# Kernel tuning notes

Measured on AMD Instinct MI355X. Metric: run time of the kernel, lower is better.

Reference implementation:

```python
import jax, jax.numpy as jnp
import numpy as np

B, N = 4, 5000


def setup_inputs() -> dict:
    key = jax.random.key(0)
    k1, k2, k3, k4 = jax.random.split(key, 4)
    param_b = jax.random.uniform(k1, (B, 1, 1), dtype=jnp.float32)
    param_g = jax.random.uniform(k2, (B, 1, 1), dtype=jnp.float32)
    mob = jax.random.uniform(k3, (B, N, N), dtype=jnp.float32)
    SIR = jax.random.uniform(k4, (B, N, 3), dtype=jnp.float32)
    return {"param_b": param_b, "param_g": param_g, "mob": mob, "SIR": SIR}


def reference(param_b, param_g, mob, SIR):
    # SIR: [B, N, 3]; mob: [B, N, N]
    S = SIR[..., 0:1]  # [B, N, 1]
    I = SIR[..., 1:2]
    R = SIR[..., 2:3]
    pop = (S + I + R)[..., 0]  # [B, N], pop_i broadcast along row i of mob
    Iv = I[..., 0]             # [B, N]
    # torch: (mob/pop * I_row).sum(1)  -> sum_i mob[b,i,j] * I_i / pop_i
    term_col = jnp.einsum('bij,bi->bj', mob, Iv / pop)
    # torch: (mob/pop * I_col).sum(2)  -> (1/pop_i) * sum_j mob[b,i,j] * I_j
    term_row = jnp.einsum('bij,bj->bi', mob, Iv) / pop
    propagation = (term_col + term_row)[..., None]  # [B, N, 1]
    I_new = param_b * propagation
    R_t = I * param_g + R
    I_t = I + I_new - I * param_g
    S_t = S - I_new
    return jnp.concatenate((I_new, S_t, I_t, R_t), axis=-1)  # [B, N, 4]
```

## Files before the change

### kernel.cpp

```cpp
#include <hip/hip_runtime.h>


constexpr int B  = 4;
constexpr int N  = 5000;
constexpr int NT = 256;
constexpr int ROWS_MAX = 80;

typedef float f32x4 __attribute__((ext_vector_type(4)));

__global__ __launch_bounds__(NT, 4) void sir_phase1(
    const float* __restrict__ mob, const float* __restrict__ SIR,
    float* __restrict__ ws_row, float* __restrict__ ws_col, int P)
{
    const int b = blockIdx.y;
    const int k = blockIdx.x;
    const int t = threadIdx.x;

    __shared__ float red[ROWS_MAX][4];

    const float* sir_b = SIR + (size_t)b * N * 3;

    f32x4 iv[5];
    #pragma unroll
    for (int kk = 0; kk < 5; ++kk) {
        const int j4 = 4 * t + 1024 * kk;
        if (kk < 4 || t < 226) {
            iv[kk][0] = sir_b[(j4 + 0) * 3 + 1];
            iv[kk][1] = sir_b[(j4 + 1) * 3 + 1];
            iv[kk][2] = sir_b[(j4 + 2) * 3 + 1];
            iv[kk][3] = sir_b[(j4 + 3) * 3 + 1];
        } else {
            iv[kk] = (f32x4)0.f;
        }
    }

    f32x4 col[5];
    #pragma unroll
    for (int kk = 0; kk < 5; ++kk) col[kk] = (f32x4)0.f;

    const float* mob_b = mob + (size_t)b * N * N;

    int r = 0;
    for (int i = k; i < N; i += P, ++r) {
        const float s  = sir_b[i * 3 + 0];
        const float ii = sir_b[i * 3 + 1];
        const float rr = sir_b[i * 3 + 2];
        const float w  = ii / (s + ii + rr);

        const float* mrow = mob_b + (size_t)i * N;
        float rp = 0.f;
        #pragma unroll
        for (int kk = 0; kk < 4; ++kk) {
            const f32x4 m = __builtin_nontemporal_load(
                reinterpret_cast<const f32x4*>(mrow + 4 * t + 1024 * kk));
            rp = fmaf(m[0], iv[kk][0], rp);
            rp = fmaf(m[1], iv[kk][1], rp);
            rp = fmaf(m[2], iv[kk][2], rp);
            rp = fmaf(m[3], iv[kk][3], rp);
            col[kk][0] = fmaf(m[0], w, col[kk][0]);
            col[kk][1] = fmaf(m[1], w, col[kk][1]);
            col[kk][2] = fmaf(m[2], w, col[kk][2]);
            col[kk][3] = fmaf(m[3], w, col[kk][3]);
        }
        if (t < 226) {
            const f32x4 m = __builtin_nontemporal_load(
                reinterpret_cast<const f32x4*>(mrow + 4 * t + 4096));
            rp = fmaf(m[0], iv[4][0], rp);
            rp = fmaf(m[1], iv[4][1], rp);
            rp = fmaf(m[2], iv[4][2], rp);
            rp = fmaf(m[3], iv[4][3], rp);
            col[4][0] = fmaf(m[0], w, col[4][0]);
            col[4][1] = fmaf(m[1], w, col[4][1]);
            col[4][2] = fmaf(m[2], w, col[4][2]);
            col[4][3] = fmaf(m[3], w, col[4][3]);
        }
        #pragma unroll
        for (int off = 32; off > 0; off >>= 1)
            rp += __shfl_xor(rp, off, 64);
        if ((t & 63) == 0) red[r][t >> 6] = rp;
    }
    __syncthreads();

    for (int q = t; q < r; q += NT) {
        const int i = k + P * q;
        ws_row[(size_t)b * N + i] = red[q][0] + red[q][1] + red[q][2] + red[q][3];
    }

    float* cp = ws_col + ((size_t)b * P + k) * N;
    #pragma unroll
    for (int kk = 0; kk < 4; ++kk)
        *reinterpret_cast<f32x4*>(cp + 4 * t + 1024 * kk) = col[kk];
    if (t < 226)
        *reinterpret_cast<f32x4*>(cp + 4 * t + 4096) = col[4];
}

__global__ __launch_bounds__(256) void sir_phase2(
    const float* __restrict__ ws_row, const float* __restrict__ ws_col,
    const float* __restrict__ SIR, const float* __restrict__ pb,
    const float* __restrict__ pg, float* __restrict__ out, int P)
{
    const int b = blockIdx.y;
    const int j = blockIdx.x * 256 + threadIdx.x;
    if (j >= N) return;

    const float* base = ws_col + (size_t)b * P * N + j;
    float cs = 0.f;
    #pragma unroll 8
    for (int p = 0; p < P; ++p) cs += base[(size_t)p * N];

    const float s  = SIR[((size_t)b * N + j) * 3 + 0];
    const float ii = SIR[((size_t)b * N + j) * 3 + 1];
    const float rr = SIR[((size_t)b * N + j) * 3 + 2];
    const float pop = s + ii + rr;
    const float tr = ws_row[(size_t)b * N + j] / pop;
    const float inew = pb[b] * (cs + tr);
    const float ig = ii * pg[b];

    f32x4 o;
    o[0] = inew;
    o[1] = s - inew;
    o[2] = ii + inew - ig;
    o[3] = ig + rr;
    *reinterpret_cast<f32x4*>(out + ((size_t)b * N + j) * 4) = o;
}

extern "C" void kernel_launch(void* const* d_in, const int* in_sizes, int n_in,
                              void* d_out, int out_size, void* d_ws, size_t ws_size,
                              hipStream_t stream)
{
    const float* pb  = (const float*)d_in[0];
    const float* pg  = (const float*)d_in[1];
    const float* mob = (const float*)d_in[2];
    const float* SIR = (const float*)d_in[3];
    float* out = (float*)d_out;
    float* ws  = (float*)d_ws;

    int P = 256;
    while (P > 64 && ((size_t)B * N + (size_t)B * P * N) * 4 > ws_size) P >>= 1;

    float* ws_row = ws;
    float* ws_col = ws + B * N;

    sir_phase1<<<dim3(P, B), NT, 0, stream>>>(mob, SIR, ws_row, ws_col, P);
    sir_phase2<<<dim3((N + 255) / 256, B), 256, 0, stream>>>(
        ws_row, ws_col, SIR, pb, pg, out, P);
}
```

Before: 515.1 us.

## Prefetch next mob row in registers and defer row reductions to after loop

Phase 1 now software-pipelines the row stream: while computing on the current row held in registers, it issues loads for the next row and its SIR values. The per-row cross-wave shuffle reduction is replaced by writing per-thread partials to a larger shared array, which all four waves reduce together after the loop. Workspace column stores and phase-2 loads become nontemporal, and the P fallback is changed to a fixed 250. The aim is to hide global-load latency in a low-occupancy, bandwidth-starved loop, at the cost of about 20 more VGPRs for the second row buffer and more LDS.

```diff
diff --git a/kernel.cpp b/kernel.cpp
--- a/kernel.cpp
+++ b/kernel.cpp
@@ -1,10 +1,10 @@
 #include <hip/hip_runtime.h>
 
 
-constexpr int B  = 4;
-constexpr int N  = 5000;
-constexpr int NT = 256;
-constexpr int ROWS_MAX = 80;
+constexpr int B    = 4;
+constexpr int N    = 5000;
+constexpr int NT   = 256;
+constexpr int ROWS = 20;
 
 typedef float f32x4 __attribute__((ext_vector_type(4)));
 
@@ -16,9 +16,10 @@
     const int k = blockIdx.x;
     const int t = threadIdx.x;
 
-    __shared__ float red[ROWS_MAX][4];
+    __shared__ float red[ROWS][NT];
 
     const float* sir_b = SIR + (size_t)b * N * 3;
+    const float* mob_b = mob + (size_t)b * N * N;
 
     f32x4 iv[5];
     #pragma unroll
@@ -38,60 +39,76 @@
     #pragma unroll
     for (int kk = 0; kk < 5; ++kk) col[kk] = (f32x4)0.f;
 
-    const float* mob_b = mob + (size_t)b * N * N;
+    f32x4 mc[5], mn[5];
+
+    {
+        const float* mrow = mob_b + (size_t)k * N;
+        #pragma unroll
+        for (int kk = 0; kk < 4; ++kk)
+            mc[kk] = __builtin_nontemporal_load(
+                reinterpret_cast<const f32x4*>(mrow + 4 * t + 1024 * kk));
+        mc[4] = (t < 226)
+            ? __builtin_nontemporal_load(reinterpret_cast<const f32x4*>(mrow + 4 * t + 4096))
+            : (f32x4)0.f;
+    }
+    float sc = sir_b[k * 3 + 0], ic = sir_b[k * 3 + 1], rc = sir_b[k * 3 + 2];
 
     int r = 0;
     for (int i = k; i < N; i += P, ++r) {
-        const float s  = sir_b[i * 3 + 0];
-        const float ii = sir_b[i * 3 + 1];
-        const float rr = sir_b[i * 3 + 2];
-        const float w  = ii / (s + ii + rr);
+        const int inext = i + P;
+        float sn = 0.f, in_ = 0.f, rn = 0.f;
+        if (inext < N) {
+            const float* mrow = mob_b + (size_t)inext * N;
+            #pragma unroll
+            for (int kk = 0; kk < 4; ++kk)
+                mn[kk] = __builtin_nontemporal_load(
+                    reinterpret_cast<const f32x4*>(mrow + 4 * t + 1024 * kk));
+            mn[4] = (t < 226)
+                ? __builtin_nontemporal_load(reinterpret_cast<const f32x4*>(mrow + 4 * t + 4096))
+                : (f32x4)0.f;
+            sn = sir_b[inext * 3 + 0];
+            in_ = sir_b[inext * 3 + 1];
+            rn = sir_b[inext * 3 + 2];
+        }
 
-        const float* mrow = mob_b + (size_t)i * N;
+        const float w = ic / (sc + ic + rc);
         float rp = 0.f;
         #pragma unroll
-        for (int kk = 0; kk < 4; ++kk) {
-            const f32x4 m = __builtin_nontemporal_load(
-                reinterpret_cast<const f32x4*>(mrow + 4 * t + 1024 * kk));
-            rp = fmaf(m[0], iv[kk][0], rp);
-            rp = fmaf(m[1], iv[kk][1], rp);
-            rp = fmaf(m[2], iv[kk][2], rp);
-            rp = fmaf(m[3], iv[kk][3], rp);
-            col[kk][0] = fmaf(m[0], w, col[kk][0]);
-            col[kk][1] = fmaf(m[1], w, col[kk][1]);
-            col[kk][2] = fmaf(m[2], w, col[kk][2]);
-            col[kk][3] = fmaf(m[3], w, col[kk][3]);
+        for (int kk = 0; kk < 5; ++kk) {
+            rp = fmaf(mc[kk][0], iv[kk][0], rp);
+            rp = fmaf(mc[kk][1], iv[kk][1], rp);
+            rp = fmaf(mc[kk][2], iv[kk][2], rp);
+            rp = fmaf(mc[kk][3], iv[kk][3], rp);
+            col[kk][0] = fmaf(mc[kk][0], w, col[kk][0]);
+            col[kk][1] = fmaf(mc[kk][1], w, col[kk][1]);
+            col[kk][2] = fmaf(mc[kk][2], w, col[kk][2]);
+            col[kk][3] = fmaf(mc[kk][3], w, col[kk][3]);
         }
-        if (t < 226) {
-            const f32x4 m = __builtin_nontemporal_load(
-                reinterpret_cast<const f32x4*>(mrow + 4 * t + 4096));
-            rp = fmaf(m[0], iv[4][0], rp);
-            rp = fmaf(m[1], iv[4][1], rp);
-            rp = fmaf(m[2], iv[4][2], rp);
-            rp = fmaf(m[3], iv[4][3], rp);
-            col[4][0] = fmaf(m[0], w, col[4][0]);
-            col[4][1] = fmaf(m[1], w, col[4][1]);
-            col[4][2] = fmaf(m[2], w, col[4][2]);
-            col[4][3] = fmaf(m[3], w, col[4][3]);
-        }
+        red[r][t] = rp;
+
         #pragma unroll
-        for (int off = 32; off > 0; off >>= 1)
-            rp += __shfl_xor(rp, off, 64);
-        if ((t & 63) == 0) red[r][t >> 6] = rp;
+        for (int kk = 0; kk < 5; ++kk) mc[kk] = mn[kk];
+        sc = sn; ic = in_; rc = rn;
     }
     __syncthreads();
 
-    for (int q = t; q < r; q += NT) {
-        const int i = k + P * q;
-        ws_row[(size_t)b * N + i] = red[q][0] + red[q][1] + red[q][2] + red[q][3];
+    const int wave = t >> 6, lane = t & 63;
+    for (int q = wave; q < r; q += 4) {
+        float v = red[q][lane] + red[q][lane + 64] + red[q][lane + 128] + red[q][lane + 192];
+        #pragma unroll
+        for (int off = 32; off > 0; off >>= 1)
+            v += __shfl_xor(v, off, 64);
+        if (lane == 0) ws_row[(size_t)b * N + k + P * q] = v;
     }
 
     float* cp = ws_col + ((size_t)b * P + k) * N;
     #pragma unroll
     for (int kk = 0; kk < 4; ++kk)
-        *reinterpret_cast<f32x4*>(cp + 4 * t + 1024 * kk) = col[kk];
+        __builtin_nontemporal_store(col[kk],
+            reinterpret_cast<f32x4*>(cp + 4 * t + 1024 * kk));
     if (t < 226)
-        *reinterpret_cast<f32x4*>(cp + 4 * t + 4096) = col[4];
+        __builtin_nontemporal_store(col[4],
+            reinterpret_cast<f32x4*>(cp + 4 * t + 4096));
 }
 
 __global__ __launch_bounds__(256) void sir_phase2(
@@ -106,7 +123,8 @@
     const float* base = ws_col + (size_t)b * P * N + j;
     float cs = 0.f;
     #pragma unroll 8
-    for (int p = 0; p < P; ++p) cs += base[(size_t)p * N];
+    for (int p = 0; p < P; ++p)
+        cs += __builtin_nontemporal_load(base + (size_t)p * N);
 
     const float s  = SIR[((size_t)b * N + j) * 3 + 0];
     const float ii = SIR[((size_t)b * N + j) * 3 + 1];
@@ -136,7 +154,7 @@
     float* ws  = (float*)d_ws;
 
     int P = 256;
-    while (P > 64 && ((size_t)B * N + (size_t)B * P * N) * 4 > ws_size) P >>= 1;
+    if (((size_t)B * N + (size_t)B * P * N) * 4 > ws_size) P = 250;
 
     float* ws_row = ws;
     float* ws_col = ws + B * N;
```

New measurement: 532.5 us. 1.03x slower.
